# Kernel tuning notes

Measured on AMD Instinct MI355X. Metric: run time of the kernel, lower is better.

The kernel has to match this reference:

```python
import jax, jax.numpy as jnp
import numpy as np

B, T, D, U = 128, 1024, 256, 256


def setup_inputs() -> dict:
    key = jax.random.key(0)
    ks = jax.random.split(key, 16)
    s_in = 1.0 / np.sqrt(D)
    s_rec = 1.0 / np.sqrt(U)
    inp = {"x": jax.random.normal(ks[0], (B, T, D), dtype=jnp.float32)}
    for i, name in enumerate(["wf", "wi", "wc", "wo"]):
        inp[name] = jax.random.normal(ks[1 + i], (D, U), dtype=jnp.float32) * s_in
    for i, name in enumerate(["rf", "ri", "rc", "ro", "pf", "pi", "po"]):
        inp[name] = jax.random.normal(ks[5 + i], (U, U), dtype=jnp.float32) * s_rec
    for i, name in enumerate(["bf", "bi", "bc", "bo"]):
        inp[name] = jax.random.normal(ks[12 + i], (U,), dtype=jnp.float32) * 0.01
    return inp


def reference(x, wf, wi, wc, wo, rf, ri, rc, ro, pf, pi, po, bf, bi, bc, bo):
    # Peephole LSTM: scan over time, state (c, h) each [B, U].
    def step(carry, xt):
        c, h = carry
        f_gate = jax.nn.sigmoid(xt @ wf + h @ rf + c @ pf + bf)
        i_gate = jax.nn.sigmoid(xt @ wi + h @ ri + c @ pi + bi)
        c_tild = jnp.tanh(xt @ wc + h @ rc + bc)
        c_new = f_gate * c + i_gate * c_tild
        o_gate = jax.nn.sigmoid(xt @ wo + h @ ro + c_new @ po + bo)
        h_new = jnp.tanh(c_new) * o_gate
        return (c_new, h_new), None

    b = x.shape[0]
    u = wf.shape[1]
    c0 = jnp.zeros((b, u), dtype=x.dtype)
    h0 = jnp.zeros((b, u), dtype=x.dtype)
    (_, h_final), _ = jax.lax.scan(step, (c0, h0), jnp.swapaxes(x, 0, 1))  # time-major [T,B,D]
    return h_final
```

## Files before the change

kernel.cpp:

```cpp
#include <hip/hip_runtime.h>

#define TT 1024
#define DU 256

#define CEX_OFF   0
#define HEX_OFF   65536
#define STMP_OFF  131072
#define TST_OFF   139264
#define GCON_OFF  172032
#define BLOB_OFF  174080
#define CHUNK_ELEMS (11*16*256)

typedef unsigned short ushort_t;
typedef unsigned u32;
typedef unsigned long long u64;
typedef __attribute__((ext_vector_type(8))) short short8;
typedef __attribute__((ext_vector_type(2))) unsigned long long u64x2;
typedef __attribute__((ext_vector_type(4))) float floatx4;

#define MFMA(a, b, c) __builtin_amdgcn_mfma_f32_16x16x32_bf16((a), (b), (c), 0, 0, 0)

__device__ __forceinline__ ushort_t f2bf(float f) {
  unsigned u = __float_as_uint(f);
  return (ushort_t)((u + 0x7fffu + ((u >> 16) & 1u)) >> 16);
}
__device__ __forceinline__ float sigf(float x) { return 1.0f / (1.0f + __expf(-x)); }
__device__ __forceinline__ float tanhf_(float x) {
  float t = 1.0f - 2.0f / (__expf(2.0f * fabsf(x)) + 1.0f);
  return copysignf(t, x);
}

__device__ __forceinline__ short8 ldfrag(const ushort_t* p) {
  union { struct { u64 a, b; } q; short8 s; } v;
  v.q.a = __hip_atomic_load((const u64*)p,       __ATOMIC_RELAXED, __HIP_MEMORY_SCOPE_AGENT);
  v.q.b = __hip_atomic_load((const u64*)(p + 4), __ATOMIC_RELAXED, __HIP_MEMORY_SCOPE_AGENT);
  return v.s;
}
__device__ __forceinline__ void wait_slow(const u32* stG, u32 tgt, int lane) {
  const u32* p = stG + (lane & 15) * 16;
  for (;;) {
    u32 s = __hip_atomic_load(p, __ATOMIC_RELAXED, __HIP_MEMORY_SCOPE_AGENT);
    if (__all((int)(s >= tgt))) return;
    __builtin_amdgcn_s_sleep(1);
  }
}

__device__ __forceinline__ u32 poll_nt(const u32* p) {
  u32 s;
  asm volatile("global_load_dword %0, %1, off nt\n\ts_waitcnt vmcnt(0)"
               : "=v"(s) : "v"(p) : "memory");
  return s;
}
__device__ __forceinline__ int wait_fast(const u32* stG, u32 tgt, int lane) {
  const u32* p = stG + (lane & 15) * 16;
  int it = 0;
  for (;;) {
    u32 s = poll_nt(p);
    if (__all((int)(s >= tgt))) return 1;
    if (++it > 16384) return 0;
    __builtin_amdgcn_s_sleep(1);
  }
}
__device__ __forceinline__ short8 ldfrag_nt(const ushort_t* p) {
  union { u64x2 q; short8 s; } v;
  v.q = __builtin_nontemporal_load((const u64x2*)p);
  return v.s;
}

__device__ int test_nt(u32* tb, int mem, int lane) {
  u64* td = (u64*)tb;
  u32* tstamp = tb + 256;
  u32* tready = tb + 512;
  int ok = 1;
  for (int r = 0; r < 3; ++r) {
    u32 seq = 1u + (u32)r;
    if (lane == 0)
      __hip_atomic_store(tready + mem, seq, __ATOMIC_RELEASE, __HIP_MEMORY_SCOPE_AGENT);
    { int it = 0;
      for (;;) {
        u32 v = __hip_atomic_load(tready + (lane & 15), __ATOMIC_RELAXED,
                                  __HIP_MEMORY_SCOPE_AGENT);
        if (__all((int)(v >= seq))) break;
        if (++it > 16384) return 0;
        __builtin_amdgcn_s_sleep(2);
      } }
    if (lane < 8) {
      u64 v = 0x9E3779B97F4A7C15ull * (u64)(seq * 131u + (u32)mem * 17u + (u32)lane + 1u);
      asm volatile("global_store_dwordx2 %0, %1, off"
                   :: "v"(td + mem * 8 + lane), "v"(v) : "memory");
    }
    asm volatile("s_waitcnt vmcnt(0)" ::: "memory");
    if (lane == 0)
      asm volatile("global_store_dword %0, %1, off"
                   :: "v"(tstamp + mem * 16), "v"(seq) : "memory");
    int saw = 0;
    { int it = 0;
      for (;;) {
        u32 s = poll_nt(tstamp + (lane & 15) * 16);
        if (__all((int)(s >= seq))) { saw = 1; break; }
        if (++it > 192) break;
        __builtin_amdgcn_s_sleep(2);
      } }
    if (!saw) { ok = 0; continue; }
    u64 a = __builtin_nontemporal_load(td + lane);
    u64 b = __builtin_nontemporal_load(td + lane + 64);
    int s0 = lane >> 3, j0 = lane & 7, s1 = (lane + 64) >> 3, j1 = (lane + 64) & 7;
    u64 e0 = 0x9E3779B97F4A7C15ull * (u64)(seq * 131u + (u32)s0 * 17u + (u32)j0 + 1u);
    u64 e1 = 0x9E3779B97F4A7C15ull * (u64)(seq * 131u + (u32)s1 * 17u + (u32)j1 + 1u);
    if (!__all((int)((a == e0) && (b == e1)))) ok = 0;
  }
  return ok;
}

__global__ void conv_weights(
    const float* __restrict__ wf, const float* __restrict__ wi,
    const float* __restrict__ wc, const float* __restrict__ wo,
    const float* __restrict__ rf, const float* __restrict__ ri,
    const float* __restrict__ rc, const float* __restrict__ ro,
    const float* __restrict__ pf, const float* __restrict__ pi,
    const float* __restrict__ po, ushort_t* __restrict__ blob)
{
  int id = blockIdx.x * 256 + threadIdx.x;
  int k   = id & 255;
  int col = (id >> 8) & 15;
  int q   = id >> 12;
  int m   = q % 11;
  int mm  = q / 11;
  const float* srcs[11] = {wf, wi, wc, wo, rf, ri, rc, ro, pf, pi, po};
  float v = srcs[m][k * 256 + mm * 16 + col];
  unsigned u = __float_as_uint(v);
  blob[id] = (ushort_t)((u + 0x7fffu + ((u >> 16) & 1u)) >> 16);
}

extern "C" __global__ void __launch_bounds__(128, 1)
lstm_rec(const float* __restrict__ x, const ushort_t* __restrict__ blob,
         ushort_t* __restrict__ h_ex, ushort_t* __restrict__ c_ex,
         u32* __restrict__ stamps, u32* __restrict__ tst, u32* __restrict__ gcon,
         const float* __restrict__ bfv, const float* __restrict__ biv,
         const float* __restrict__ bcv, const float* __restrict__ bov,
         float* __restrict__ out)
{
  __shared__ ushort_t xa[16 * 264];
  __shared__ float pre[4][16][17];
  __shared__ float pop[16][17];
  __shared__ float bia[4][16];
  __shared__ int s_mode;

  const int tid = threadIdx.x;
  const int bid = blockIdx.x;
  const int wv = tid >> 6;
  const int lane = tid & 63;
  const int lr = lane & 15;
  const int lk = lane >> 4;

  const int grp = bid & 7;
  const int mem = bid >> 3;
  const int gb0 = grp * 16;
  const int gc0 = mem * 16;

  u32* gok  = gcon;
  u32* gpol = gcon + 256;

  if (wv == 0) {
    __builtin_amdgcn_fence(__ATOMIC_ACQUIRE, "agent");
    int okv = test_nt(tst + grp * 1024, mem, lane);
    if (lane == 0)
      __hip_atomic_store(gok + bid, 1u | ((u32)okv << 1),
                         __ATOMIC_RELEASE, __HIP_MEMORY_SCOPE_AGENT);
    if (bid == 0) {
      u32 pol = 0; int it = 0;
      for (;;) {
        u32 a = __hip_atomic_load(gok + lane, __ATOMIC_RELAXED, __HIP_MEMORY_SCOPE_AGENT);
        u32 b = __hip_atomic_load(gok + 64 + lane, __ATOMIC_RELAXED, __HIP_MEMORY_SCOPE_AGENT);
        if (__all((int)((a & 1u) && (b & 1u)))) {
          pol = __all((int)(((a >> 1) & 1u) && ((b >> 1) & 1u))) ? 1u : 0u;
          break;
        }
        if (++it > 32768) { pol = 0; break; }
        __builtin_amdgcn_s_sleep(4);
      }
      if (lane == 0)
        __hip_atomic_store(gpol, pol + 1u, __ATOMIC_RELEASE, __HIP_MEMORY_SCOPE_AGENT);
    }
    u32 p;
    for (;;) {
      p = __hip_atomic_load(gpol, __ATOMIC_RELAXED, __HIP_MEMORY_SCOPE_AGENT);
      if (p) break;
      __builtin_amdgcn_s_sleep(4);
    }
    if (lane == 0) s_mode = (int)(p - 1u);
  }
  __syncthreads();
  const int fast = s_mode;
  int wedged = 0;
  if (fast) __builtin_amdgcn_fence(__ATOMIC_ACQUIRE, "agent");

  const ushort_t* wb = blob + (size_t)mem * CHUNK_ELEMS;
  short8 wXa[8], wXb[8], wRa[8], wRb[8], wPa[8], wPb[8];
  {
    const int m0 = wv ? 2 : 0;
    const int p0 = wv ? 10 : 8;
    const int p1 = wv ? 10 : 9;
#pragma unroll
    for (int s = 0; s < 8; ++s) {
      const int ko = s * 32 + lk * 8;
      wXa[s] = *(const short8*)(wb + ((m0    ) * 16 + lr) * 256 + ko);
      wXb[s] = *(const short8*)(wb + ((m0 + 1) * 16 + lr) * 256 + ko);
      wRa[s] = *(const short8*)(wb + ((m0 + 4) * 16 + lr) * 256 + ko);
      wRb[s] = *(const short8*)(wb + ((m0 + 5) * 16 + lr) * 256 + ko);
      wPa[s] = *(const short8*)(wb + (p0 * 16 + lr) * 256 + ko);
      wPb[s] = *(const short8*)(wb + (p1 * 16 + lr) * 256 + ko);
    }
  }

  if (tid < 64) {
    const float* bs = (tid < 16) ? bfv : (tid < 32) ? biv : (tid < 48) ? bcv : bov;
    bia[tid >> 4][tid & 15] = bs[gc0 + (tid & 15)];
  }
  const int pb = tid >> 3, pc = (tid & 7) * 2;
  float cr0 = 0.f, cr1 = 0.f;

  const int xr = tid >> 3, xc = (tid & 7) * 32;
  {
    const float* xp = x + (size_t)(gb0 + xr) * TT * DU + xc;
#pragma unroll
    for (int u = 0; u < 8; ++u) {
      float4 f = *(const float4*)(xp + u * 4);
      *(u64*)&xa[xr * 264 + xc + u * 4] =
          (u64)f2bf(f.x) | ((u64)f2bf(f.y) << 16) |
          ((u64)f2bf(f.z) << 32) | ((u64)f2bf(f.w) << 48);
    }
  }
  __syncthreads();

  const floatx4 z4 = {0.f, 0.f, 0.f, 0.f};
  floatx4 accA = z4, accB = z4;
#pragma unroll
  for (int s = 0; s < 8; ++s) {
    short8 a = *(const short8*)&xa[lr * 264 + s * 32 + lk * 8];
    accA = MFMA(a, wXa[s], accA);
    accB = MFMA(a, wXb[s], accB);
  }

  u32* stG = stamps + grp * 256;
  ushort_t* cG = c_ex + grp * 16 * 256;
  ushort_t* hG = h_ex + grp * 16 * 256;
  u32* cSlot = (u32*)(cG + mem * 256 + pb * 16 + pc);
  u32* hSlot = (u32*)(hG + mem * 256 + pb * 16 + pc);

  for (int t = 0; t < TT; ++t) {
    if (t > 0) {
      if (fast) { if (!wedged && !wait_fast(stG, 2u * (u32)t, lane)) wedged = 1; }
      else wait_slow(stG, 2u * (u32)t, lane);
    }
    if (t > 0) {
      short8 hf[8];
#pragma unroll
      for (int s = 0; s < 8; ++s) {
        int k = s * 32 + lk * 8;
        hf[s] = fast ? ldfrag_nt(hG + (k >> 4) * 256 + lr * 16 + (k & 15))
                     : ldfrag(hG + (k >> 4) * 256 + lr * 16 + (k & 15));
      }
      float4 xf[8];
      if (t < TT - 1) {
        const float* xp = x + ((size_t)(gb0 + xr) * TT + (t + 1)) * DU + xc;
#pragma unroll
        for (int u = 0; u < 8; ++u) xf[u] = *(const float4*)(xp + u * 4);
      }
#pragma unroll
      for (int s = 0; s < 8; ++s) {
        accA = MFMA(hf[s], wRa[s], accA);
        accB = MFMA(hf[s], wRb[s], accB);
      }
#pragma unroll
      for (int r = 0; r < 4; ++r) {
        pre[wv * 2    ][lk * 4 + r][lr] = accA[r];
        pre[wv * 2 + 1][lk * 4 + r][lr] = accB[r];
      }
      __syncthreads();
      {
        float fg = sigf(pre[0][pb][pc] + bia[0][pc]);
        float ig = sigf(pre[1][pb][pc] + bia[1][pc]);
        float ct = tanhf_(pre[2][pb][pc] + bia[2][pc]);
        cr0 = fg * cr0 + ig * ct;
        fg = sigf(pre[0][pb][pc + 1] + bia[0][pc + 1]);
        ig = sigf(pre[1][pb][pc + 1] + bia[1][pc + 1]);
        ct = tanhf_(pre[2][pb][pc + 1] + bia[2][pc + 1]);
        cr1 = fg * cr1 + ig * ct;
      }
      u32 cw = (u32)f2bf(cr0) | ((u32)f2bf(cr1) << 16);
      if (fast)
        asm volatile("global_store_dword %0, %1, off" :: "v"(cSlot), "v"(cw) : "memory");
      else
        __hip_atomic_store(cSlot, cw, __ATOMIC_RELAXED, __HIP_MEMORY_SCOPE_AGENT);
      asm volatile("s_waitcnt vmcnt(0)" ::: "memory");
      __syncthreads();
      if (tid == 0) {
        u32 sv = 2u * (u32)t + 1u;
        if (fast)
          asm volatile("global_store_dword %0, %1, off" :: "v"(stG + mem * 16), "v"(sv) : "memory");
        else
          __hip_atomic_store(stG + mem * 16, sv, __ATOMIC_RELAXED, __HIP_MEMORY_SCOPE_AGENT);
      }
      if (t < TT - 1) {
#pragma unroll
        for (int u = 0; u < 8; ++u) {
          float4 f = xf[u];
          *(u64*)&xa[xr * 264 + xc + u * 4] =
              (u64)f2bf(f.x) | ((u64)f2bf(f.y) << 16) |
              ((u64)f2bf(f.z) << 32) | ((u64)f2bf(f.w) << 48);
        }
        __syncthreads();
      }
    } else {
      float4 xf[8];
      {
        const float* xp = x + ((size_t)(gb0 + xr) * TT + 1) * DU + xc;
#pragma unroll
        for (int u = 0; u < 8; ++u) xf[u] = *(const float4*)(xp + u * 4);
      }
#pragma unroll
      for (int r = 0; r < 4; ++r) {
        pre[wv * 2    ][lk * 4 + r][lr] = accA[r];
        pre[wv * 2 + 1][lk * 4 + r][lr] = accB[r];
      }
      __syncthreads();
      {
        float fg = sigf(pre[0][pb][pc] + bia[0][pc]);
        float ig = sigf(pre[1][pb][pc] + bia[1][pc]);
        float ct = tanhf_(pre[2][pb][pc] + bia[2][pc]);
        cr0 = fg * cr0 + ig * ct;
        fg = sigf(pre[0][pb][pc + 1] + bia[0][pc + 1]);
        ig = sigf(pre[1][pb][pc + 1] + bia[1][pc + 1]);
        ct = tanhf_(pre[2][pb][pc + 1] + bia[2][pc + 1]);
        cr1 = fg * cr1 + ig * ct;
      }
      u32 cw = (u32)f2bf(cr0) | ((u32)f2bf(cr1) << 16);
      if (fast)
        asm volatile("global_store_dword %0, %1, off" :: "v"(cSlot), "v"(cw) : "memory");
      else
        __hip_atomic_store(cSlot, cw, __ATOMIC_RELAXED, __HIP_MEMORY_SCOPE_AGENT);
      asm volatile("s_waitcnt vmcnt(0)" ::: "memory");
      __syncthreads();
      if (tid == 0) {
        u32 sv = 1u;
        if (fast)
          asm volatile("global_store_dword %0, %1, off" :: "v"(stG + mem * 16), "v"(sv) : "memory");
        else
          __hip_atomic_store(stG + mem * 16, sv, __ATOMIC_RELAXED, __HIP_MEMORY_SCOPE_AGENT);
      }
#pragma unroll
      for (int u = 0; u < 8; ++u) {
        float4 f = xf[u];
        *(u64*)&xa[xr * 264 + xc + u * 4] =
            (u64)f2bf(f.x) | ((u64)f2bf(f.y) << 16) |
            ((u64)f2bf(f.z) << 32) | ((u64)f2bf(f.w) << 48);
      }
      __syncthreads();
    }

    if (fast) { if (!wedged && !wait_fast(stG, 2u * (u32)t + 1u, lane)) wedged = 1; }
    else wait_slow(stG, 2u * (u32)t + 1u, lane);

    {
      short8 cf[8];
#pragma unroll
      for (int s = 0; s < 8; ++s) {
        int k = s * 32 + lk * 8;
        cf[s] = fast ? ldfrag_nt(cG + (k >> 4) * 256 + lr * 16 + (k & 15))
                     : ldfrag(cG + (k >> 4) * 256 + lr * 16 + (k & 15));
      }
      if (wv == 0) {
        accA = z4; accB = z4;
#pragma unroll
        for (int s = 0; s < 8; ++s) {
          accA = MFMA(cf[s], wPa[s], accA);
          accB = MFMA(cf[s], wPb[s], accB);
        }
      } else {
        floatx4 pacc = z4;
#pragma unroll
        for (int s = 0; s < 8; ++s)
          pacc = MFMA(cf[s], wPa[s], pacc);
#pragma unroll
        for (int r = 0; r < 4; ++r) pop[lk * 4 + r][lr] = pacc[r];
      }
    }
    __syncthreads();

    float og0 = sigf(pre[3][pb][pc] + pop[pb][pc] + bia[3][pc]);
    float hv0 = tanhf_(cr0) * og0;
    float og1 = sigf(pre[3][pb][pc + 1] + pop[pb][pc + 1] + bia[3][pc + 1]);
    float hv1 = tanhf_(cr1) * og1;
    if (t == TT - 1) {
      float2 o2; o2.x = hv0; o2.y = hv1;
      *(float2*)&out[(gb0 + pb) * 256 + gc0 + pc] = o2;
      break;
    }
    u32 hw = (u32)f2bf(hv0) | ((u32)f2bf(hv1) << 16);
    if (fast)
      asm volatile("global_store_dword %0, %1, off" :: "v"(hSlot), "v"(hw) : "memory");
    else
      __hip_atomic_store(hSlot, hw, __ATOMIC_RELAXED, __HIP_MEMORY_SCOPE_AGENT);
    asm volatile("s_waitcnt vmcnt(0)" ::: "memory");
    __syncthreads();
    if (tid == 0) {
      u32 sv = 2u * (u32)t + 2u;
      if (fast)
        asm volatile("global_store_dword %0, %1, off" :: "v"(stG + mem * 16), "v"(sv) : "memory");
      else
        __hip_atomic_store(stG + mem * 16, sv, __ATOMIC_RELAXED, __HIP_MEMORY_SCOPE_AGENT);
    }

    if (wv == 1) { accA = z4; accB = z4; }
#pragma unroll
    for (int s = 0; s < 8; ++s) {
      short8 a = *(const short8*)&xa[lr * 264 + s * 32 + lk * 8];
      accA = MFMA(a, wXa[s], accA);
      accB = MFMA(a, wXb[s], accB);
    }
  }
}

extern "C" void kernel_launch(void* const* d_in, const int* in_sizes, int n_in,
                              void* d_out, int out_size, void* d_ws, size_t ws_size,
                              hipStream_t stream) {
  const float* x   = (const float*)d_in[0];
  const float* bfv = (const float*)d_in[12];
  const float* biv = (const float*)d_in[13];
  const float* bcv = (const float*)d_in[14];
  const float* bov = (const float*)d_in[15];
  float* outp = (float*)d_out;

  char* ws = (char*)d_ws;
  ushort_t* c_exp = (ushort_t*)(ws + CEX_OFF);
  ushort_t* h_exp = (ushort_t*)(ws + HEX_OFF);
  u32* stmp = (u32*)(ws + STMP_OFF);
  u32* tstp = (u32*)(ws + TST_OFF);
  u32* gcon = (u32*)(ws + GCON_OFF);
  ushort_t* blob = (ushort_t*)(ws + BLOB_OFF);

  hipMemsetAsync(d_ws, 0, BLOB_OFF, stream);

  hipLaunchKernelGGL(conv_weights, dim3(2816), dim3(256), 0, stream,
                     (const float*)d_in[1], (const float*)d_in[2],
                     (const float*)d_in[3], (const float*)d_in[4],
                     (const float*)d_in[5], (const float*)d_in[6],
                     (const float*)d_in[7], (const float*)d_in[8],
                     (const float*)d_in[9], (const float*)d_in[10],
                     (const float*)d_in[11], blob);

  hipLaunchKernelGGL(lstm_rec, dim3(128), dim3(128), 0, stream,
                     x, (const ushort_t*)blob, h_exp, c_exp, stmp, tstp, gcon,
                     bfv, biv, bcv, bov, outp);
}
```

Before: 3.690 ms.

## Use per-wave publish flags instead of block barriers and drop poll sleep

After: 3.338 ms. 1.11x faster.

```diff
diff --git a/kernel.cpp b/kernel.cpp
--- a/kernel.cpp
+++ b/kernel.cpp
@@ -37,7 +37,7 @@
   return v.s;
 }
 __device__ __forceinline__ void wait_slow(const u32* stG, u32 tgt, int lane) {
-  const u32* p = stG + (lane & 15) * 16;
+  const u32* p = stG + (lane & 15) * 16 + ((lane >> 4) & 1);
   for (;;) {
     u32 s = __hip_atomic_load(p, __ATOMIC_RELAXED, __HIP_MEMORY_SCOPE_AGENT);
     if (__all((int)(s >= tgt))) return;
@@ -52,13 +52,12 @@
   return s;
 }
 __device__ __forceinline__ int wait_fast(const u32* stG, u32 tgt, int lane) {
-  const u32* p = stG + (lane & 15) * 16;
+  const u32* p = stG + (lane & 15) * 16 + ((lane >> 4) & 1);
   int it = 0;
   for (;;) {
     u32 s = poll_nt(p);
     if (__all((int)(s >= tgt))) return 1;
     if (++it > 16384) return 0;
-    __builtin_amdgcn_s_sleep(1);
   }
 }
 __device__ __forceinline__ short8 ldfrag_nt(const ushort_t* p) {
@@ -247,13 +246,12 @@
   ushort_t* hG = h_ex + grp * 16 * 256;
   u32* cSlot = (u32*)(cG + mem * 256 + pb * 16 + pc);
   u32* hSlot = (u32*)(hG + mem * 256 + pb * 16 + pc);
+  u32* mySt  = stG + mem * 16 + wv;
 
   for (int t = 0; t < TT; ++t) {
     if (t > 0) {
       if (fast) { if (!wedged && !wait_fast(stG, 2u * (u32)t, lane)) wedged = 1; }
       else wait_slow(stG, 2u * (u32)t, lane);
-    }
-    if (t > 0) {
       short8 hf[8];
 #pragma unroll
       for (int s = 0; s < 8; ++s) {
@@ -261,94 +259,50 @@
         hf[s] = fast ? ldfrag_nt(hG + (k >> 4) * 256 + lr * 16 + (k & 15))
                      : ldfrag(hG + (k >> 4) * 256 + lr * 16 + (k & 15));
       }
-      float4 xf[8];
-      if (t < TT - 1) {
-        const float* xp = x + ((size_t)(gb0 + xr) * TT + (t + 1)) * DU + xc;
-#pragma unroll
-        for (int u = 0; u < 8; ++u) xf[u] = *(const float4*)(xp + u * 4);
-      }
 #pragma unroll
       for (int s = 0; s < 8; ++s) {
         accA = MFMA(hf[s], wRa[s], accA);
         accB = MFMA(hf[s], wRb[s], accB);
       }
-#pragma unroll
-      for (int r = 0; r < 4; ++r) {
-        pre[wv * 2    ][lk * 4 + r][lr] = accA[r];
-        pre[wv * 2 + 1][lk * 4 + r][lr] = accB[r];
-      }
-      __syncthreads();
-      {
-        float fg = sigf(pre[0][pb][pc] + bia[0][pc]);
-        float ig = sigf(pre[1][pb][pc] + bia[1][pc]);
-        float ct = tanhf_(pre[2][pb][pc] + bia[2][pc]);
-        cr0 = fg * cr0 + ig * ct;
-        fg = sigf(pre[0][pb][pc + 1] + bia[0][pc + 1]);
-        ig = sigf(pre[1][pb][pc + 1] + bia[1][pc + 1]);
-        ct = tanhf_(pre[2][pb][pc + 1] + bia[2][pc + 1]);
-        cr1 = fg * cr1 + ig * ct;
-      }
+    }
+#pragma unroll
+    for (int r = 0; r < 4; ++r) {
+      pre[wv * 2    ][lk * 4 + r][lr] = accA[r];
+      pre[wv * 2 + 1][lk * 4 + r][lr] = accB[r];
+    }
+    __syncthreads();
+
+    {
+      float fg = sigf(pre[0][pb][pc] + bia[0][pc]);
+      float ig = sigf(pre[1][pb][pc] + bia[1][pc]);
+      float ct = tanhf_(pre[2][pb][pc] + bia[2][pc]);
+      cr0 = fg * cr0 + ig * ct;
+      fg = sigf(pre[0][pb][pc + 1] + bia[0][pc + 1]);
+      ig = sigf(pre[1][pb][pc + 1] + bia[1][pc + 1]);
+      ct = tanhf_(pre[2][pb][pc + 1] + bia[2][pc + 1]);
+      cr1 = fg * cr1 + ig * ct;
+    }
+    {
       u32 cw = (u32)f2bf(cr0) | ((u32)f2bf(cr1) << 16);
       if (fast)
         asm volatile("global_store_dword %0, %1, off" :: "v"(cSlot), "v"(cw) : "memory");
       else
         __hip_atomic_store(cSlot, cw, __ATOMIC_RELAXED, __HIP_MEMORY_SCOPE_AGENT);
       asm volatile("s_waitcnt vmcnt(0)" ::: "memory");
-      __syncthreads();
-      if (tid == 0) {
+      if (lane == 0) {
         u32 sv = 2u * (u32)t + 1u;
         if (fast)
-          asm volatile("global_store_dword %0, %1, off" :: "v"(stG + mem * 16), "v"(sv) : "memory");
+          asm volatile("global_store_dword %0, %1, off" :: "v"(mySt), "v"(sv) : "memory");
         else
-          __hip_atomic_store(stG + mem * 16, sv, __ATOMIC_RELAXED, __HIP_MEMORY_SCOPE_AGENT);
-      }
-      if (t < TT - 1) {
-#pragma unroll
-        for (int u = 0; u < 8; ++u) {
-          float4 f = xf[u];
-          *(u64*)&xa[xr * 264 + xc + u * 4] =
-              (u64)f2bf(f.x) | ((u64)f2bf(f.y) << 16) |
-              ((u64)f2bf(f.z) << 32) | ((u64)f2bf(f.w) << 48);
-        }
-        __syncthreads();
-      }
-    } else {
+          __hip_atomic_store(mySt, sv, __ATOMIC_RELAXED, __HIP_MEMORY_SCOPE_AGENT);
+      }
+    }
+
+    if (t < TT - 1) {
       float4 xf[8];
-      {
-        const float* xp = x + ((size_t)(gb0 + xr) * TT + 1) * DU + xc;
-#pragma unroll
-        for (int u = 0; u < 8; ++u) xf[u] = *(const float4*)(xp + u * 4);
-      }
-#pragma unroll
-      for (int r = 0; r < 4; ++r) {
-        pre[wv * 2    ][lk * 4 + r][lr] = accA[r];
-        pre[wv * 2 + 1][lk * 4 + r][lr] = accB[r];
-      }
-      __syncthreads();
-      {
-        float fg = sigf(pre[0][pb][pc] + bia[0][pc]);
-        float ig = sigf(pre[1][pb][pc] + bia[1][pc]);
-        float ct = tanhf_(pre[2][pb][pc] + bia[2][pc]);
-        cr0 = fg * cr0 + ig * ct;
-        fg = sigf(pre[0][pb][pc + 1] + bia[0][pc + 1]);
-        ig = sigf(pre[1][pb][pc + 1] + bia[1][pc + 1]);
-        ct = tanhf_(pre[2][pb][pc + 1] + bia[2][pc + 1]);
-        cr1 = fg * cr1 + ig * ct;
-      }
-      u32 cw = (u32)f2bf(cr0) | ((u32)f2bf(cr1) << 16);
-      if (fast)
-        asm volatile("global_store_dword %0, %1, off" :: "v"(cSlot), "v"(cw) : "memory");
-      else
-        __hip_atomic_store(cSlot, cw, __ATOMIC_RELAXED, __HIP_MEMORY_SCOPE_AGENT);
-      asm volatile("s_waitcnt vmcnt(0)" ::: "memory");
-      __syncthreads();
-      if (tid == 0) {
-        u32 sv = 1u;
-        if (fast)
-          asm volatile("global_store_dword %0, %1, off" :: "v"(stG + mem * 16), "v"(sv) : "memory");
-        else
-          __hip_atomic_store(stG + mem * 16, sv, __ATOMIC_RELAXED, __HIP_MEMORY_SCOPE_AGENT);
-      }
+      const float* xp = x + ((size_t)(gb0 + xr) * TT + (t + 1)) * DU + xc;
+#pragma unroll
+      for (int u = 0; u < 8; ++u) xf[u] = *(const float4*)(xp + u * 4);
 #pragma unroll
       for (int u = 0; u < 8; ++u) {
         float4 f = xf[u];
@@ -397,19 +351,20 @@
       *(float2*)&out[(gb0 + pb) * 256 + gc0 + pc] = o2;
       break;
     }
-    u32 hw = (u32)f2bf(hv0) | ((u32)f2bf(hv1) << 16);
-    if (fast)
-      asm volatile("global_store_dword %0, %1, off" :: "v"(hSlot), "v"(hw) : "memory");
-    else
-      __hip_atomic_store(hSlot, hw, __ATOMIC_RELAXED, __HIP_MEMORY_SCOPE_AGENT);
-    asm volatile("s_waitcnt vmcnt(0)" ::: "memory");
-    __syncthreads();
-    if (tid == 0) {
-      u32 sv = 2u * (u32)t + 2u;
+    {
+      u32 hw = (u32)f2bf(hv0) | ((u32)f2bf(hv1) << 16);
       if (fast)
-        asm volatile("global_store_dword %0, %1, off" :: "v"(stG + mem * 16), "v"(sv) : "memory");
+        asm volatile("global_store_dword %0, %1, off" :: "v"(hSlot), "v"(hw) : "memory");
       else
-        __hip_atomic_store(stG + mem * 16, sv, __ATOMIC_RELAXED, __HIP_MEMORY_SCOPE_AGENT);
+        __hip_atomic_store(hSlot, hw, __ATOMIC_RELAXED, __HIP_MEMORY_SCOPE_AGENT);
+      asm volatile("s_waitcnt vmcnt(0)" ::: "memory");
+      if (lane == 0) {
+        u32 sv = 2u * (u32)t + 2u;
+        if (fast)
+          asm volatile("global_store_dword %0, %1, off" :: "v"(mySt), "v"(sv) : "memory");
+        else
+          __hip_atomic_store(mySt, sv, __ATOMIC_RELAXED, __HIP_MEMORY_SCOPE_AGENT);
+      }
     }
 
     if (wv == 1) { accA = z4; accB = z4; }
```
